# Performance work log

Hardware: AMD Instinct MI355X
Metric: run time of the kernel (lower is better)

Reference implementation:

```python
import jax, jax.numpy as jnp
import numpy as np

D = 512
H = 8
DH = D // H


def setup_inputs() -> dict:
    key = jax.random.key(0)
    ks = jax.random.split(key, 6)
    B, S = 2, 4096
    scale = 1.0 / np.sqrt(D)
    x = jax.random.normal(ks[0], (B, S, D), dtype=jnp.float32)
    W_q = jax.random.normal(ks[1], (D, D), dtype=jnp.float32) * scale
    W_k = jax.random.normal(ks[2], (D, D), dtype=jnp.float32) * scale
    W_v = jax.random.normal(ks[3], (D, D), dtype=jnp.float32) * scale
    W_proj = jax.random.normal(ks[4], (D, D), dtype=jnp.float32) * scale
    b_proj = jax.random.normal(ks[5], (D,), dtype=jnp.float32) * 0.01
    return {"x": x, "W_q": W_q, "W_k": W_k, "W_v": W_v,
            "W_proj": W_proj, "b_proj": b_proj}


def reference(x, W_q, W_k, W_v, W_proj, b_proj):
    B, S, _ = x.shape
    # torch Linear: y = x @ W.T
    def proj(W):
        y = jnp.einsum('bsd,ed->bse', x, W)
        return y.reshape(B, S, H, DH).transpose(0, 2, 1, 3)  # [B,H,S,DH]
    q, k, v = proj(W_q), proj(W_k), proj(W_v)
    scores = jnp.einsum('bhqd,bhkd->bhqk', q, k) / np.sqrt(DH)  # [B,H,S,S]
    causal = jnp.tril(jnp.ones((S, S), dtype=bool))
    neg = jnp.finfo(scores.dtype).min
    scores = jnp.where(causal[None, None, :, :], scores, neg)
    w = jax.nn.softmax(scores, axis=-1)
    attn = jnp.einsum('bhqk,bhkd->bhqd', w, v)  # [B,H,S,DH]
    attn = attn.transpose(0, 2, 1, 3).reshape(B, S, D)
    return jnp.einsum('bsd,ed->bse', attn, W_proj) + b_proj
```

## Files before the change

kernel.cpp:

```cpp
#include <hip/hip_runtime.h>
#include <hip/hip_bf16.h>
#include <stdint.h>

#define D_MODEL 512
#define NH 8
#define DH 64
#define SEQ 4096
#define NBH 16

typedef __attribute__((ext_vector_type(8))) short bf16x8;
typedef __attribute__((ext_vector_type(4))) float f32x4;
typedef __attribute__((ext_vector_type(16))) float f32x16;

#define CSCALE 0.18033688011112042f

__device__ __forceinline__ uint32_t pkbf(float a, float b) {
    uint32_t r;
    asm("v_cvt_pk_bf16_f32 %0, %1, %2" : "=v"(r) : "v"(a), "v"(b));
    return r;
}

#define SWZ(R) (((R) + ((R) >> 2)) & 3)

__device__ __forceinline__ bf16x8 cvt8(float4 u, float4 v, float s) {
    union { uint32_t w[4]; bf16x8 h; } r;
    r.w[0] = pkbf(u.x * s, u.y * s); r.w[1] = pkbf(u.z * s, u.w * s);
    r.w[2] = pkbf(v.x * s, v.y * s); r.w[3] = pkbf(v.z * s, v.w * s);
    return r.h;
}

__global__ __launch_bounds__(256) void qkv_kernel(
    const float* __restrict__ x,
    const float* __restrict__ Wq, const float* __restrict__ Wk,
    const float* __restrict__ Wv,
    short* __restrict__ Qb, short* __restrict__ Kb, short* __restrict__ Vt)
{
    __shared__ __align__(16) short at[2][4096];
    __shared__ __align__(16) short bt[2][4096];

    const int tid  = threadIdx.x;
    const int wave = tid >> 6;
    const int lane = tid & 63;
    const int ln = lane & 15, quad = lane >> 4;
    const int z = blockIdx.z;
    const float* W = (z == 0) ? Wq : (z == 1) ? Wk : Wv;
    const float wscale = (z == 0) ? CSCALE : 1.0f;
    const int m0 = blockIdx.x * 128;
    const int n0 = blockIdx.y * 128;
    const int mh = (wave & 1) * 64, nh = (wave >> 1) * 64;

    const int ck0 = tid, ck1 = tid + 256;
    const int R0 = ck0 >> 2, R1 = ck1 >> 2;
    const int c0 = (ck0 & 3) ^ SWZ(R0), c1 = (ck1 & 3) ^ SWZ(R1);

    float4 ra[4], rb[4];
    auto loadAB = [&](int kc) {
        const float* pa0 = x + (size_t)(m0 + R0) * D_MODEL + kc + c0 * 8;
        const float* pa1 = x + (size_t)(m0 + R1) * D_MODEL + kc + c1 * 8;
        ra[0] = *(const float4*)pa0; ra[1] = *(const float4*)(pa0 + 4);
        ra[2] = *(const float4*)pa1; ra[3] = *(const float4*)(pa1 + 4);
        const float* pb0 = W + (size_t)(n0 + R0) * D_MODEL + kc + c0 * 8;
        const float* pb1 = W + (size_t)(n0 + R1) * D_MODEL + kc + c1 * 8;
        rb[0] = *(const float4*)pb0; rb[1] = *(const float4*)(pb0 + 4);
        rb[2] = *(const float4*)pb1; rb[3] = *(const float4*)(pb1 + 4);
    };
    auto writeAB = [&](int buf) {
        *(bf16x8*)&at[buf][ck0 * 8] = cvt8(ra[0], ra[1], 1.0f);
        *(bf16x8*)&at[buf][ck1 * 8] = cvt8(ra[2], ra[3], 1.0f);
        *(bf16x8*)&bt[buf][ck0 * 8] = cvt8(rb[0], rb[1], wscale);
        *(bf16x8*)&bt[buf][ck1 * 8] = cvt8(rb[2], rb[3], wscale);
    };

    f32x4 acc[4][4] = {};

    loadAB(0);
    writeAB(0);

    for (int s = 0; s < 16; ++s) {
        const int cur = s & 1;
        __syncthreads();
        if (s < 15) loadAB((s + 1) * 32);

        bf16x8 a[4], b[4];
#pragma unroll
        for (int i = 0; i < 4; ++i) {
            const int R = mh + i * 16 + ln;
            a[i] = *(const bf16x8*)(&at[cur][R * 32 + ((quad ^ SWZ(R)) * 8)]);
        }
#pragma unroll
        for (int j = 0; j < 4; ++j) {
            const int R = nh + j * 16 + ln;
            b[j] = *(const bf16x8*)(&bt[cur][R * 32 + ((quad ^ SWZ(R)) * 8)]);
        }
#pragma unroll
        for (int i = 0; i < 4; ++i)
#pragma unroll
            for (int j = 0; j < 4; ++j)
                acc[i][j] = __builtin_amdgcn_mfma_f32_16x16x32_bf16(
                    a[i], b[j], acc[i][j], 0, 0, 0);

        if (s < 15) writeAB(cur ^ 1);
    }

    if (z == 2) {
#pragma unroll
        for (int i = 0; i < 4; ++i) {
            const int row0 = m0 + mh + i * 16 + quad * 4;
            const int bb = row0 >> 12, sq = row0 & (SEQ - 1);
#pragma unroll
            for (int j = 0; j < 4; ++j) {
                const int n = n0 + nh + j * 16 + ln;
                const int h = n >> 6, dh = n & 63;
                uint2 st;
                st.x = pkbf(acc[i][j][0], acc[i][j][1]);
                st.y = pkbf(acc[i][j][2], acc[i][j][3]);
                *(uint2*)(Vt + (size_t)((bb * NH + h) * DH + dh) * SEQ + sq) = st;
            }
        }
    } else {
        short* P = (z == 0) ? Qb : Kb;
#pragma unroll
        for (int i = 0; i < 4; ++i)
#pragma unroll
            for (int j = 0; j < 4; ++j) {
                const int n = n0 + nh + j * 16 + ln;
                const int h = n >> 6, dh = n & 63;
                const uint32_t lo = pkbf(acc[i][j][0], acc[i][j][1]);
                const uint32_t hi2 = pkbf(acc[i][j][2], acc[i][j][3]);
#pragma unroll
                for (int r = 0; r < 4; ++r) {
                    const int row = m0 + mh + i * 16 + quad * 4 + r;
                    const int bb = row >> 12, sq = row & (SEQ - 1);
                    const uint32_t w = (r < 2) ? lo : hi2;
                    P[((size_t)((bb * NH + h) * SEQ + sq) << 6) + dh] =
                        (short)((r & 1) ? (w >> 16) : (w & 0xffff));
                }
            }
    }
}

__global__ __launch_bounds__(256) void attn_kernel(
    const short* __restrict__ Qb, const short* __restrict__ Kb,
    const short* __restrict__ Vt, short* __restrict__ ao)
{
    __shared__ __align__(16) short kt[2][4096];
    __shared__ __align__(16) short vt[2][4096];

    const int tid  = threadIdx.x;
    const int wave = tid >> 6;
    const int lane = tid & 63;
    const int l31 = lane & 31, hi = lane >> 5;
    const int bh = blockIdx.y;
    const int w_ = (blockIdx.x + 4 * bh) & 31;
    const int g2 = ((bh >> 3) & 1) ? (31 - w_) : w_;
    const short* Qp = Qb + (size_t)bh * SEQ * DH;
    const short* Kp = Kb + (size_t)bh * SEQ * DH;
    const short* Vp = Vt + (size_t)bh * DH * SEQ;
    const int bb = bh >> 3, h = bh & 7;
    const int q0 = g2 * 128 + wave * 32;
    const int myq = q0 + l31;
    const int jdiag = q0 >> 6;
    const int jmax = 2 * g2 + 1;

    const int ckA = tid, ckB = tid + 256;
    const int RA = ckA >> 3, RB = ckB >> 3;
    const int cA = (ckA & 7) ^ (RA & 7), cB = (ckB & 7) ^ (RB & 7);
    const int RA31 = RA & 31, RB31 = RB & 31;
    const int kkA = (RA & 32) + ((RA31 & 8) << 1) + ((RA31 & 4) << 1)
                  + ((RA31 & 16) >> 2) + (RA31 & 3);
    const int kkB = (RB & 32) + ((RB31 & 8) << 1) + ((RB31 & 4) << 1)
                  + ((RB31 & 16) >> 2) + (RB31 & 3);
    const size_t kOffA = ((size_t)kkA << 6) + cA * 8;
    const size_t kOffB = ((size_t)kkB << 6) + cB * 8;
    const size_t vOffA = (size_t)RA * SEQ + cA * 8;
    const size_t vOffB = (size_t)RB * SEQ + cB * 8;

    bf16x8 sk0, sk1, sv0, sv1;
    auto load_tile = [&](int j) {
        const size_t k0 = (size_t)j * 64;
        sk0 = *(const bf16x8*)(Kp + (k0 << 6) + kOffA);
        sk1 = *(const bf16x8*)(Kp + (k0 << 6) + kOffB);
        sv0 = *(const bf16x8*)(Vp + vOffA + k0);
        sv1 = *(const bf16x8*)(Vp + vOffB + k0);
    };
    auto write_tile = [&](int buf) {
        *(bf16x8*)&kt[buf][ckA * 8] = sk0;
        *(bf16x8*)&kt[buf][ckB * 8] = sk1;
        *(bf16x8*)&vt[buf][ckA * 8] = sv0;
        *(bf16x8*)&vt[buf][ckB * 8] = sv1;
    };

    bf16x8 qf[4];
#pragma unroll
    for (int c = 0; c < 4; ++c)
        qf[c] = *(const bf16x8*)(Qp + (size_t)myq * DH + c * 16 + hi * 8);

    const bf16x8 ones = { (short)0x3F80, (short)0x3F80, (short)0x3F80,
                          (short)0x3F80, (short)0x3F80, (short)0x3F80,
                          (short)0x3F80, (short)0x3F80 };

    f32x16 o0 = {}, o1 = {};
    f32x16 lacc = {};

    load_tile(0);
    write_tile(0);
    load_tile(1);
    __syncthreads();

    for (int j = 0; j <= jmax; ++j) {
        const int cur = j & 1;
        if (j < jmax) {
            write_tile(cur ^ 1);
            if (j + 1 < jmax) load_tile(j + 2);
        }

        f32x16 s0 = {}, s1 = {};
        const int sw = l31 & 7;
#pragma unroll
        for (int c = 0; c < 4; ++c) {
            const int pc = ((2 * c + hi) ^ sw) * 8;
            bf16x8 a0 = *(const bf16x8*)(&kt[cur][l31 * 64 + pc]);
            bf16x8 a1 = *(const bf16x8*)(&kt[cur][(32 + l31) * 64 + pc]);
            s0 = __builtin_amdgcn_mfma_f32_32x32x16_bf16(a0, qf[c], s0, 0, 0, 0);
            s1 = __builtin_amdgcn_mfma_f32_32x32x16_bf16(a1, qf[c], s1, 0, 0, 0);
        }
        if (j >= jdiag) {
            const int k0 = j * 64;
#pragma unroll
            for (int reg = 0; reg < 16; ++reg) {
                const int kl = ((reg >> 2) & 1) * 16 + hi * 8
                             + ((reg >> 3) & 1) * 4 + (reg & 3);
                if (k0 + kl > myq)      s0[reg] = -3e38f;
                if (k0 + 32 + kl > myq) s1[reg] = -3e38f;
            }
        }
#pragma unroll
        for (int i = 0; i < 16; ++i) {
            s0[i] = __builtin_amdgcn_exp2f(s0[i]);
            s1[i] = __builtin_amdgcn_exp2f(s1[i]);
        }

        union { uint32_t u[4]; bf16x8 v; } p00, p01, p10, p11;
        p00.u[0] = pkbf(s0[0], s0[1]);   p00.u[1] = pkbf(s0[2], s0[3]);
        p00.u[2] = pkbf(s0[8], s0[9]);   p00.u[3] = pkbf(s0[10], s0[11]);
        p01.u[0] = pkbf(s0[4], s0[5]);   p01.u[1] = pkbf(s0[6], s0[7]);
        p01.u[2] = pkbf(s0[12], s0[13]); p01.u[3] = pkbf(s0[14], s0[15]);
        p10.u[0] = pkbf(s1[0], s1[1]);   p10.u[1] = pkbf(s1[2], s1[3]);
        p10.u[2] = pkbf(s1[8], s1[9]);   p10.u[3] = pkbf(s1[10], s1[11]);
        p11.u[0] = pkbf(s1[4], s1[5]);   p11.u[1] = pkbf(s1[6], s1[7]);
        p11.u[2] = pkbf(s1[12], s1[13]); p11.u[3] = pkbf(s1[14], s1[15]);

        lacc = __builtin_amdgcn_mfma_f32_32x32x16_bf16(ones, p00.v, lacc, 0, 0, 0);
        lacc = __builtin_amdgcn_mfma_f32_32x32x16_bf16(ones, p01.v, lacc, 0, 0, 0);
        lacc = __builtin_amdgcn_mfma_f32_32x32x16_bf16(ones, p10.v, lacc, 0, 0, 0);
        lacc = __builtin_amdgcn_mfma_f32_32x32x16_bf16(ones, p11.v, lacc, 0, 0, 0);

        {
            const short* vrow = &vt[cur][l31 * 64];
            bf16x8 v00 = *(const bf16x8*)(vrow + (((0 + hi) ^ sw) * 8));
            bf16x8 v01 = *(const bf16x8*)(vrow + (((2 + hi) ^ sw) * 8));
            bf16x8 v10 = *(const bf16x8*)(vrow + (((4 + hi) ^ sw) * 8));
            bf16x8 v11 = *(const bf16x8*)(vrow + (((6 + hi) ^ sw) * 8));
            o0 = __builtin_amdgcn_mfma_f32_32x32x16_bf16(v00, p00.v, o0, 0, 0, 0);
            o0 = __builtin_amdgcn_mfma_f32_32x32x16_bf16(v01, p01.v, o0, 0, 0, 0);
            o0 = __builtin_amdgcn_mfma_f32_32x32x16_bf16(v10, p10.v, o0, 0, 0, 0);
            o0 = __builtin_amdgcn_mfma_f32_32x32x16_bf16(v11, p11.v, o0, 0, 0, 0);
        }
        {
            const short* vrow = &vt[cur][(32 + l31) * 64];
            bf16x8 v00 = *(const bf16x8*)(vrow + (((0 + hi) ^ sw) * 8));
            bf16x8 v01 = *(const bf16x8*)(vrow + (((2 + hi) ^ sw) * 8));
            bf16x8 v10 = *(const bf16x8*)(vrow + (((4 + hi) ^ sw) * 8));
            bf16x8 v11 = *(const bf16x8*)(vrow + (((6 + hi) ^ sw) * 8));
            o1 = __builtin_amdgcn_mfma_f32_32x32x16_bf16(v00, p00.v, o1, 0, 0, 0);
            o1 = __builtin_amdgcn_mfma_f32_32x32x16_bf16(v01, p01.v, o1, 0, 0, 0);
            o1 = __builtin_amdgcn_mfma_f32_32x32x16_bf16(v10, p10.v, o1, 0, 0, 0);
            o1 = __builtin_amdgcn_mfma_f32_32x32x16_bf16(v11, p11.v, o1, 0, 0, 0);
        }
        __syncthreads();
    }
    const float inv = 1.0f / lacc[0];
    short* orow = ao + (size_t)(bb * SEQ + myq) * D_MODEL + h * DH;
#pragma unroll
    for (int c = 0; c < 4; ++c) {
        uint2 st;
        st.x = pkbf(o0[4 * c] * inv,     o0[4 * c + 1] * inv);
        st.y = pkbf(o0[4 * c + 2] * inv, o0[4 * c + 3] * inv);
        *(uint2*)(orow + 8 * c + 4 * hi) = st;
    }
#pragma unroll
    for (int c = 0; c < 4; ++c) {
        uint2 st;
        st.x = pkbf(o1[4 * c] * inv,     o1[4 * c + 1] * inv);
        st.y = pkbf(o1[4 * c + 2] * inv, o1[4 * c + 3] * inv);
        *(uint2*)(orow + 32 + 8 * c + 4 * hi) = st;
    }
}

__global__ __launch_bounds__(256) void proj_kernel(
    const short* __restrict__ attn, const float* __restrict__ Wp,
    const float* __restrict__ bias, float* __restrict__ out)
{
    __shared__ __align__(16) short at[2][2048];
    __shared__ __align__(16) short bt[2][4096];

    const int tid  = threadIdx.x;
    const int wave = tid >> 6;
    const int lane = tid & 63;
    const int ln = lane & 15, quad = lane >> 4;
    const int m0 = blockIdx.x * 64;
    const int n0 = blockIdx.y * 128;
    const int mh = (wave & 1) * 32, nh = (wave >> 1) * 64;

    const int RA = tid >> 2, cAc = (tid & 3) ^ SWZ(RA);
    const int ck0 = tid, ck1 = tid + 256;
    const int R0 = ck0 >> 2, R1 = ck1 >> 2;
    const int c0 = (ck0 & 3) ^ SWZ(R0), c1 = (ck1 & 3) ^ SWZ(R1);

    bf16x8 raA;
    float4 rb[4];
    auto loadAB = [&](int kc) {
        raA = *(const bf16x8*)(attn + (size_t)(m0 + RA) * D_MODEL + kc + cAc * 8);
        const float* pb0 = Wp + (size_t)(n0 + R0) * D_MODEL + kc + c0 * 8;
        const float* pb1 = Wp + (size_t)(n0 + R1) * D_MODEL + kc + c1 * 8;
        rb[0] = *(const float4*)pb0; rb[1] = *(const float4*)(pb0 + 4);
        rb[2] = *(const float4*)pb1; rb[3] = *(const float4*)(pb1 + 4);
    };
    auto writeAB = [&](int buf) {
        *(bf16x8*)&at[buf][tid * 8] = raA;
        *(bf16x8*)&bt[buf][ck0 * 8] = cvt8(rb[0], rb[1], 1.0f);
        *(bf16x8*)&bt[buf][ck1 * 8] = cvt8(rb[2], rb[3], 1.0f);
    };

    f32x4 acc[2][4] = {};

    loadAB(0);
    writeAB(0);

    for (int s = 0; s < 16; ++s) {
        const int cur = s & 1;
        __syncthreads();
        if (s < 15) loadAB((s + 1) * 32);

        bf16x8 a[2], b[4];
#pragma unroll
        for (int i = 0; i < 2; ++i) {
            const int R = mh + i * 16 + ln;
            a[i] = *(const bf16x8*)(&at[cur][R * 32 + ((quad ^ SWZ(R)) * 8)]);
        }
#pragma unroll
        for (int j = 0; j < 4; ++j) {
            const int R = nh + j * 16 + ln;
            b[j] = *(const bf16x8*)(&bt[cur][R * 32 + ((quad ^ SWZ(R)) * 8)]);
        }
#pragma unroll
        for (int i = 0; i < 2; ++i)
#pragma unroll
            for (int j = 0; j < 4; ++j)
                acc[i][j] = __builtin_amdgcn_mfma_f32_16x16x32_bf16(
                    a[i], b[j], acc[i][j], 0, 0, 0);

        if (s < 15) writeAB(cur ^ 1);
    }
#pragma unroll
    for (int j = 0; j < 4; ++j) {
        const int n = n0 + nh + j * 16 + ln;
        const float bv = bias[n];
#pragma unroll
        for (int i = 0; i < 2; ++i)
#pragma unroll
            for (int r = 0; r < 4; ++r) {
                const int row = m0 + mh + i * 16 + quad * 4 + r;
                out[(size_t)row * D_MODEL + n] = acc[i][j][r] + bv;
            }
    }
}

extern "C" void kernel_launch(void* const* d_in, const int* in_sizes, int n_in,
                              void* d_out, int out_size, void* d_ws, size_t ws_size,
                              hipStream_t stream) {
    const float* x  = (const float*)d_in[0];
    const float* Wq = (const float*)d_in[1];
    const float* Wk = (const float*)d_in[2];
    const float* Wv = (const float*)d_in[3];
    const float* Wp = (const float*)d_in[4];
    const float* bp = (const float*)d_in[5];
    float* out = (float*)d_out;

    short* Qb = (short*)d_ws;
    short* Kb = Qb + (size_t)NBH * SEQ * DH;
    short* Vt = Kb + (size_t)NBH * SEQ * DH;
    short* ab = Vt + (size_t)NBH * SEQ * DH;

    qkv_kernel<<<dim3(64, 4, 3), 256, 0, stream>>>(x, Wq, Wk, Wv, Qb, Kb, Vt);
    attn_kernel<<<dim3(32, NBH), 256, 0, stream>>>(Qb, Kb, Vt, ab);
    proj_kernel<<<dim3(128, 4), 256, 0, stream>>>(ab, Wp, bp, out);
}
```

Before: 177.9 us.

## Split attention KV range across two blocks and merge with a combine kernel

Splits each query block's key/value tiles into two halves handled by separate blocks (grid z=2). Each half writes unnormalized fp16 partial outputs and row sums, scaled by a fixed constant. A new combine kernel adds the two halves, normalizes, and writes the bf16 attention output. The aim is to double block-level parallelism so the attention kernel fills the GPU better. The cost is an extra launch and extra partial traffic, and the partials are staged in the output buffer. Correctness relies on the unchanged softmax formulation not using a running max, so the halves can be summed directly.

```diff
diff --git a/kernel.cpp b/kernel.cpp
--- a/kernel.cpp
+++ b/kernel.cpp
@@ -11,8 +11,11 @@
 typedef __attribute__((ext_vector_type(8))) short bf16x8;
 typedef __attribute__((ext_vector_type(4))) float f32x4;
 typedef __attribute__((ext_vector_type(16))) float f32x16;
+typedef __attribute__((ext_vector_type(4))) _Float16 f16x4;
+typedef __attribute__((ext_vector_type(8))) _Float16 f16x8v;
 
 #define CSCALE 0.18033688011112042f
+#define PSC 0.015625f
 
 __device__ __forceinline__ uint32_t pkbf(float a, float b) {
     uint32_t r;
@@ -141,7 +144,8 @@
 
 __global__ __launch_bounds__(256) void attn_kernel(
     const short* __restrict__ Qb, const short* __restrict__ Kb,
-    const short* __restrict__ Vt, short* __restrict__ ao)
+    const short* __restrict__ Vt, _Float16* __restrict__ po,
+    float* __restrict__ lw)
 {
     __shared__ __align__(16) short kt[2][4096];
     __shared__ __align__(16) short vt[2][4096];
@@ -151,16 +155,17 @@
     const int lane = tid & 63;
     const int l31 = lane & 31, hi = lane >> 5;
     const int bh = blockIdx.y;
+    const int z  = blockIdx.z;
     const int w_ = (blockIdx.x + 4 * bh) & 31;
     const int g2 = ((bh >> 3) & 1) ? (31 - w_) : w_;
     const short* Qp = Qb + (size_t)bh * SEQ * DH;
     const short* Kp = Kb + (size_t)bh * SEQ * DH;
     const short* Vp = Vt + (size_t)bh * DH * SEQ;
-    const int bb = bh >> 3, h = bh & 7;
     const int q0 = g2 * 128 + wave * 32;
     const int myq = q0 + l31;
     const int jdiag = q0 >> 6;
-    const int jmax = 2 * g2 + 1;
+    const int ntile = g2 + 1;
+    const int jlo = z * ntile;
 
     const int ckA = tid, ckB = tid + 256;
     const int RA = ckA >> 3, RB = ckB >> 3;
@@ -202,16 +207,17 @@
     f32x16 o0 = {}, o1 = {};
     f32x16 lacc = {};
 
-    load_tile(0);
+    load_tile(jlo);
     write_tile(0);
-    load_tile(1);
+    if (ntile > 1) load_tile(jlo + 1);
     __syncthreads();
 
-    for (int j = 0; j <= jmax; ++j) {
-        const int cur = j & 1;
-        if (j < jmax) {
+    for (int t = 0; t < ntile; ++t) {
+        const int j = jlo + t;
+        const int cur = t & 1;
+        if (t + 1 < ntile) {
             write_tile(cur ^ 1);
-            if (j + 1 < jmax) load_tile(j + 2);
+            if (t + 2 < ntile) load_tile(jlo + t + 2);
         }
 
         f32x16 s0 = {}, s1 = {};
@@ -279,22 +285,54 @@
         }
         __syncthreads();
     }
-    const float inv = 1.0f / lacc[0];
-    short* orow = ao + (size_t)(bb * SEQ + myq) * D_MODEL + h * DH;
+
+    if (hi == 0)
+        lw[(((size_t)z * NBH + bh) << 12) + myq] = lacc[0] * PSC;
+    _Float16* prow = po + (((size_t)(z * NBH + bh) * SEQ) + myq) * DH;
 #pragma unroll
     for (int c = 0; c < 4; ++c) {
-        uint2 st;
-        st.x = pkbf(o0[4 * c] * inv,     o0[4 * c + 1] * inv);
-        st.y = pkbf(o0[4 * c + 2] * inv, o0[4 * c + 3] * inv);
-        *(uint2*)(orow + 8 * c + 4 * hi) = st;
+        f16x4 st = { (_Float16)(o0[4 * c] * PSC),     (_Float16)(o0[4 * c + 1] * PSC),
+                     (_Float16)(o0[4 * c + 2] * PSC), (_Float16)(o0[4 * c + 3] * PSC) };
+        *(f16x4*)(prow + 8 * c + 4 * hi) = st;
     }
 #pragma unroll
     for (int c = 0; c < 4; ++c) {
-        uint2 st;
-        st.x = pkbf(o1[4 * c] * inv,     o1[4 * c + 1] * inv);
-        st.y = pkbf(o1[4 * c + 2] * inv, o1[4 * c + 3] * inv);
-        *(uint2*)(orow + 32 + 8 * c + 4 * hi) = st;
-    }
+        f16x4 st = { (_Float16)(o1[4 * c] * PSC),     (_Float16)(o1[4 * c + 1] * PSC),
+                     (_Float16)(o1[4 * c + 2] * PSC), (_Float16)(o1[4 * c + 3] * PSC) };
+        *(f16x4*)(prow + 32 + 8 * c + 4 * hi) = st;
+    }
+}
+
+__global__ __launch_bounds__(256) void combine_kernel(
+    const _Float16* __restrict__ po, const float* __restrict__ lw,
+    short* __restrict__ ao)
+{
+    const int t = blockIdx.x * 256 + threadIdx.x;
+    const int r = t >> 2, part = t & 3;
+    const int bh = r >> 12, q = r & 4095;
+    const int dh0 = part * 16;
+    const float l0 = lw[r];
+    const float l1 = lw[(NBH << 12) + r];
+    const float inv = 1.0f / (l0 + l1);
+    const _Float16* p0 = po + (((size_t)r) << 6) + dh0;
+    const _Float16* p1 = po + (((size_t)(r + (NBH << 12))) << 6) + dh0;
+    f16x8v a0 = *(const f16x8v*)p0;
+    f16x8v a1 = *(const f16x8v*)(p0 + 8);
+    f16x8v b0 = *(const f16x8v*)p1;
+    f16x8v b1 = *(const f16x8v*)(p1 + 8);
+    const int bb = bh >> 3, h = bh & 7;
+    short* orow = ao + (size_t)(bb * SEQ + q) * D_MODEL + h * DH + dh0;
+    uint4 w0, w1;
+    w0.x = pkbf(((float)a0[0] + (float)b0[0]) * inv, ((float)a0[1] + (float)b0[1]) * inv);
+    w0.y = pkbf(((float)a0[2] + (float)b0[2]) * inv, ((float)a0[3] + (float)b0[3]) * inv);
+    w0.z = pkbf(((float)a0[4] + (float)b0[4]) * inv, ((float)a0[5] + (float)b0[5]) * inv);
+    w0.w = pkbf(((float)a0[6] + (float)b0[6]) * inv, ((float)a0[7] + (float)b0[7]) * inv);
+    w1.x = pkbf(((float)a1[0] + (float)b1[0]) * inv, ((float)a1[1] + (float)b1[1]) * inv);
+    w1.y = pkbf(((float)a1[2] + (float)b1[2]) * inv, ((float)a1[3] + (float)b1[3]) * inv);
+    w1.z = pkbf(((float)a1[4] + (float)b1[4]) * inv, ((float)a1[5] + (float)b1[5]) * inv);
+    w1.w = pkbf(((float)a1[6] + (float)b1[6]) * inv, ((float)a1[7] + (float)b1[7]) * inv);
+    *(uint4*)orow = w0;
+    *(uint4*)(orow + 8) = w1;
 }
 
 __global__ __launch_bounds__(256) void proj_kernel(
@@ -391,8 +429,12 @@
     short* Kb = Qb + (size_t)NBH * SEQ * DH;
     short* Vt = Kb + (size_t)NBH * SEQ * DH;
     short* ab = Vt + (size_t)NBH * SEQ * DH;
+    float* lw = (float*)(ab + (size_t)NBH * SEQ * DH);
+
+    _Float16* po = (_Float16*)d_out;
 
     qkv_kernel<<<dim3(64, 4, 3), 256, 0, stream>>>(x, Wq, Wk, Wv, Qb, Kb, Vt);
-    attn_kernel<<<dim3(32, NBH), 256, 0, stream>>>(Qb, Kb, Vt, ab);
+    attn_kernel<<<dim3(32, NBH, 2), 256, 0, stream>>>(Qb, Kb, Vt, po, lw);
+    combine_kernel<<<dim3(1024), 256, 0, stream>>>(po, lw, ab);
     proj_kernel<<<dim3(128, 4), 256, 0, stream>>>(ab, Wp, bp, out);
 }
```

New measurement: 197.7 us. 1.11x slower.
